# Optimization experiments

Measured on AMD Instinct MI355X. Metric: run time of the kernel, lower is better.

Reference implementation:

```python
import jax, jax.numpy as jnp
import numpy as np

NEG_BIG = -9e15

def setup_inputs() -> dict:
    key = jax.random.key(0)
    k1, k2, k3, k4 = jax.random.split(key, 4)
    B, N, C, D = 8, 2048, 128, 128
    x = jax.random.normal(k1, (B, N, C), dtype=jnp.float32)
    adj = jax.random.randint(k2, (N, N), 0, 2, dtype=jnp.int32)
    W = jax.random.normal(k3, (D, C), dtype=jnp.float32) * (1.0 / np.sqrt(C))
    a = jax.random.normal(k4, (1, 2 * D), dtype=jnp.float32) * (1.0 / np.sqrt(2 * D))
    return {"x": x, "adj": adj, "W": W, "a": a}

def reference(x, adj, W, a):
    # Wh: [B,N,D]
    Wh = jnp.einsum('bnc,dc->bnd', x, W)
    D = Wh.shape[-1]
    a1, a2 = a[0, :D], a[0, D:]
    # e[b,i,j] = leakyrelu(a1.Wh_i + a2.Wh_j)  (algebraic split of cat([Wh_i,Wh_j]) @ a)
    f1 = Wh @ a1  # [B,N]
    f2 = Wh @ a2  # [B,N]
    e = jax.nn.leaky_relu(f1[:, :, None] + f2[:, None, :], negative_slope=0.2)  # [B,N,N]
    e = jnp.where(adj[None] > 0, e, NEG_BIG)
    attention = jax.nn.softmax(e, axis=-1)
    h_prime = jnp.einsum('bij,bjd->bid', attention, Wh)
    return jax.nn.elu(h_prime)
```

## Files before the change

kernel.cpp:

```cpp
#include <hip/hip_runtime.h>
#include <hip/hip_bf16.h>
#include <math.h>

#define BB 8
#define NN 2048
#define CC 128
#define DD 128

typedef __attribute__((ext_vector_type(8))) short short8;
typedef __attribute__((ext_vector_type(4))) float f32x4;

static __device__ __forceinline__ unsigned short f2bf(float f) {
    __hip_bfloat16 h = __float2bfloat16(f);
    return *reinterpret_cast<unsigned short*>(&h);
}
static __device__ __forceinline__ float bf2f(unsigned short u) {
    __hip_bfloat16 h = *reinterpret_cast<__hip_bfloat16*>(&u);
    return __bfloat162float(h);
}

#define PACKB 256
__global__ __launch_bounds__(256) void prep_wh_kernel(
    const int* __restrict__ adj, unsigned int* __restrict__ padj,
    const float* __restrict__ x, const float* __restrict__ W,
    const float* __restrict__ a,
    unsigned short* __restrict__ WhbT,
    float* __restrict__ f1, float* __restrict__ E2g, float* __restrict__ G2g)
{
    __shared__ unsigned short Whs[128 * 136];
    __shared__ unsigned short Wls[128 * 136];
    const int bx  = blockIdx.x;
    const int tid = threadIdx.x;

    if (bx < PACKB) {
        const int wid = bx * 256 + tid;
        #pragma unroll
        for (int rep = 0; rep < 2; ++rep) {
            const int word = wid + rep * 65536;
            const int4* src = (const int4*)adj + (size_t)word * 8;
            unsigned int m = 0;
            #pragma unroll
            for (int k = 0; k < 8; ++k) {
                int4 v = src[k];
                m |= (v.x > 0 ? 1u : 0u) << (k * 4);
                m |= (v.y > 0 ? 1u : 0u) << (k * 4 + 1);
                m |= (v.z > 0 ? 1u : 0u) << (k * 4 + 2);
                m |= (v.w > 0 ? 1u : 0u) << (k * 4 + 3);
            }
            padj[word] = m;
        }
        return;
    }

    const int g  = bx - PACKB;
    const int b  = g & 7;
    const int n0 = (g >> 3) * 64;

    #pragma unroll
    for (int k = 0; k < 16; ++k) {
        const int e   = tid + 256 * k;
        float4 wv = *(const float4*)&W[e * 4];
        const int row = e >> 5;
        const int col = (e & 31) * 4;
        ushort4 hv, lv;
        hv.x = f2bf(wv.x); lv.x = f2bf(wv.x - bf2f(hv.x));
        hv.y = f2bf(wv.y); lv.y = f2bf(wv.y - bf2f(hv.y));
        hv.z = f2bf(wv.z); lv.z = f2bf(wv.z - bf2f(hv.z));
        hv.w = f2bf(wv.w); lv.w = f2bf(wv.w - bf2f(hv.w));
        *(ushort4*)&Whs[row * 136 + col] = hv;
        *(ushort4*)&Wls[row * 136 + col] = lv;
    }
    __syncthreads();

    const int w    = tid >> 6;
    const int lane = tid & 63;
    const int fr   = lane & 15, fk = lane >> 4;
    const int n    = n0 + w * 16 + fr;

    short8 bh[4], bl[4];
    const float* xrow = &x[((size_t)(b * NN) + n) * CC];
    #pragma unroll
    for (int ks = 0; ks < 4; ++ks) {
        float xv[8];
        *(float4*)&xv[0] = *(const float4*)&xrow[(ks * 4 + fk) * 8];
        *(float4*)&xv[4] = *(const float4*)&xrow[(ks * 4 + fk) * 8 + 4];
        #pragma unroll
        for (int e = 0; e < 8; ++e) {
            unsigned short h = f2bf(xv[e]);
            bh[ks][e] = (short)h;
            bl[ks][e] = (short)f2bf(xv[e] - bf2f(h));
        }
    }

    f32x4 acc[8];
    #pragma unroll
    for (int dt = 0; dt < 8; ++dt) acc[dt] = (f32x4){0.f, 0.f, 0.f, 0.f};

    #pragma unroll
    for (int dt = 0; dt < 8; ++dt) {
        #pragma unroll
        for (int ks = 0; ks < 4; ++ks) {
            const int off = (dt * 16 + fr) * 136 + (ks * 4 + fk) * 8;
            short8 aH = *(const short8*)&Whs[off];
            short8 aL = *(const short8*)&Wls[off];
            acc[dt] = __builtin_amdgcn_mfma_f32_16x16x32_bf16(aH, bh[ks], acc[dt], 0, 0, 0);
            acc[dt] = __builtin_amdgcn_mfma_f32_16x16x32_bf16(aH, bl[ks], acc[dt], 0, 0, 0);
            acc[dt] = __builtin_amdgcn_mfma_f32_16x16x32_bf16(aL, bh[ks], acc[dt], 0, 0, 0);
        }
    }

    float p1 = 0.f, p2 = 0.f;
    #pragma unroll
    for (int dt = 0; dt < 8; ++dt) {
        #pragma unroll
        for (int r = 0; r < 4; ++r) {
            const int d = dt * 16 + fk * 4 + r;
            p1 += acc[dt][r] * a[d];
            p2 += acc[dt][r] * a[DD + d];
        }
    }
    p1 += __shfl_xor(p1, 16); p1 += __shfl_xor(p1, 32);
    p2 += __shfl_xor(p2, 16); p2 += __shfl_xor(p2, 32);
    if (fk == 0) {
        f1[b * NN + n]  = p1;
        E2g[b * NN + n] = __expf(p2);
        G2g[b * NN + n] = __expf(0.2f * p2);
    }

    #pragma unroll
    for (int dt = 0; dt < 8; ++dt) {
        #pragma unroll
        for (int r = 0; r < 4; ++r) {
            const int d = dt * 16 + fk * 4 + r;
            WhbT[((size_t)(b * 128 + d)) * NN + n] = f2bf(acc[dt][r]);
        }
    }
}

__global__ __launch_bounds__(512) void gat_kernel(
    const unsigned short* __restrict__ WhbT,
    const unsigned int* __restrict__ padj,
    const float* __restrict__ f1,
    const float* __restrict__ E2g, const float* __restrict__ G2g,
    float* __restrict__ out)
{
    constexpr int NC = NN / 64;
    __shared__ __align__(16) unsigned char smem[66048];
    unsigned short* Bs0 = (unsigned short*)smem;
    unsigned short* Bs1 = (unsigned short*)(smem + 16384);
    unsigned short* Ps0 = (unsigned short*)(smem + 32768);
    unsigned short* Ps1 = (unsigned short*)(smem + 40960);
    float* E2s  = (float*)(smem + 49152);
    float* G2s  = (float*)(smem + 57344);
    float* Srow = (float*)(smem + 65536);
    float* Sred = (float*)(smem + 65792);
    float* T    = (float*)smem;

    const int tid  = threadIdx.x;
    const int gblk = blockIdx.x;
    const int b    = gblk & 7;
    const int i0   = (gblk >> 3) * 64;

    #pragma unroll
    for (int k = 0; k < NN / 512; ++k) {
        E2s[tid + 512 * k] = E2g[b * NN + tid + 512 * k];
        G2s[tid + 512 * k] = G2g[b * NN + tid + 512 * k];
    }

    const int prow = tid >> 3;
    const int pjb  = tid & 7;
    const float f1r = f1[b * NN + i0 + prow];
    const float E1r = __expf(f1r);
    const float G1r = __expf(0.2f * f1r);
    const int psw = ((pjb ^ (prow & 7)) << 3);
    const unsigned int* padjRow = padj + (size_t)(i0 + prow) * 64;

    const int w    = tid >> 6;
    const int wr   = w >> 2, wc = w & 3;
    const int lane = tid & 63;
    const int fr   = lane & 15;
    const int fk   = lane >> 4;
    f32x4 acc00 = {0.f,0.f,0.f,0.f}, acc01 = {0.f,0.f,0.f,0.f};
    f32x4 acc10 = {0.f,0.f,0.f,0.f}, acc11 = {0.f,0.f,0.f,0.f};
    float s_part = 0.f;

    const size_t wbase = (size_t)b * 128 * NN;
    const int g0 = tid,       gd0 = g0 >> 3, gj0 = (g0 & 7) * 8;
    const int g1 = tid + 512, gd1 = g1 >> 3, gj1 = (g1 & 7) * 8;
    const int sw0 = gd0 * 64 + ((((g0) & 7) ^ (gd0 & 7)) << 3);
    const int sw1 = gd1 * 64 + ((((g1) & 7) ^ (gd1 & 7)) << 3);

    uint4 brA0, brA1, brB0, brB1;
    unsigned int pwA, pwB;

#define LOADSET(s, c) do {                                                   \
        br##s##0 = *(const uint4*)&WhbT[wbase + (size_t)gd0 * NN + (c) * 64 + gj0]; \
        br##s##1 = *(const uint4*)&WhbT[wbase + (size_t)gd1 * NN + (c) * 64 + gj1]; \
        pw##s    = padjRow[(c) * 2 + (pjb >> 2)];                            \
    } while (0)

#define PSTAGE(Bsb, Psb, s, c) do {                                          \
        float4 eA = *(const float4*)&E2s[(c) * 64 + pjb * 8];                \
        float4 eB = *(const float4*)&E2s[(c) * 64 + pjb * 8 + 4];            \
        float4 gA = *(const float4*)&G2s[(c) * 64 + pjb * 8];                \
        float4 gB = *(const float4*)&G2s[(c) * 64 + pjb * 8 + 4];            \
        float ev[8], gv[8];                                                  \
        *(float4*)&ev[0] = eA; *(float4*)&ev[4] = eB;                        \
        *(float4*)&gv[0] = gA; *(float4*)&gv[4] = gB;                        \
        unsigned int pbits = (pw##s >> ((pjb & 3) << 3)) & 0xffu;            \
        unsigned short pks[8];                                               \
        float ssum = 0.f;                                                    \
        _Pragma("unroll")                                                    \
        for (int e = 0; e < 8; ++e) {                                        \
            float mv = E1r * ev[e];                                          \
            float gg = G1r * gv[e];                                          \
            float wv = fmaxf(mv, gg);                                        \
            wv = ((pbits >> e) & 1u) ? wv : 0.f;                             \
            unsigned short bw = f2bf(wv);                                    \
            pks[e] = bw;                                                     \
            ssum += bf2f(bw);                                                \
        }                                                                    \
        s_part += ssum;                                                      \
        *(uint4*)&Bsb[sw0] = br##s##0;                                       \
        *(uint4*)&Bsb[sw1] = br##s##1;                                       \
        uint4 pv;                                                            \
        pv.x = (unsigned int)pks[0] | ((unsigned int)pks[1] << 16);          \
        pv.y = (unsigned int)pks[2] | ((unsigned int)pks[3] << 16);          \
        pv.z = (unsigned int)pks[4] | ((unsigned int)pks[5] << 16);          \
        pv.w = (unsigned int)pks[6] | ((unsigned int)pks[7] << 16);          \
        *(uint4*)&Psb[prow * 64 + psw] = pv;                                 \
    } while (0)

#define MFMAC(Bsb, Psb) do {                                                 \
        __builtin_amdgcn_s_setprio(1);                                       \
        _Pragma("unroll")                                                    \
        for (int ks = 0; ks < 2; ++ks) {                                     \
            const int jbl = ks * 4 + fk;                                     \
            const int sb  = ((jbl ^ (fr & 7)) << 3);                         \
            short8 aF0 = *(const short8*)&Psb[(wr * 32 + fr) * 64 + sb];     \
            short8 aF1 = *(const short8*)&Psb[(wr * 32 + 16 + fr) * 64 + sb];\
            short8 bF0 = *(const short8*)&Bsb[(wc * 32 + fr) * 64 + sb];     \
            short8 bF1 = *(const short8*)&Bsb[(wc * 32 + 16 + fr) * 64 + sb];\
            acc00 = __builtin_amdgcn_mfma_f32_16x16x32_bf16(aF0, bF0, acc00, 0, 0, 0); \
            acc01 = __builtin_amdgcn_mfma_f32_16x16x32_bf16(aF0, bF1, acc01, 0, 0, 0); \
            acc10 = __builtin_amdgcn_mfma_f32_16x16x32_bf16(aF1, bF0, acc10, 0, 0, 0); \
            acc11 = __builtin_amdgcn_mfma_f32_16x16x32_bf16(aF1, bF1, acc11, 0, 0, 0); \
        }                                                                    \
        __builtin_amdgcn_s_setprio(0);                                       \
    } while (0)

    LOADSET(A, 0);
    __syncthreads();
    PSTAGE(Bs0, Ps0, A, 0);
    LOADSET(B, 1);
    __syncthreads();

    #pragma unroll 1
    for (int cc = 0; cc < NC; cc += 2) {
        PSTAGE(Bs1, Ps1, B, cc + 1);
        if (cc + 2 < NC) LOADSET(A, cc + 2);
        MFMAC(Bs0, Ps0);
        __syncthreads();
        if (cc + 2 < NC) PSTAGE(Bs0, Ps0, A, cc + 2);
        if (cc + 3 < NC) LOADSET(B, cc + 3);
        MFMAC(Bs1, Ps1);
        __syncthreads();
    }

#undef LOADSET
#undef PSTAGE
#undef MFMAC

    {
        float v = s_part;
        v += __shfl_xor(v, 1); v += __shfl_xor(v, 2); v += __shfl_xor(v, 4);
        if (pjb == 0) Srow[prow] = v;
    }
    __syncthreads();
    if (tid < 64) Sred[tid] = 1.0f / Srow[tid];
    __syncthreads();

    #pragma unroll
    for (int it = 0; it < 2; ++it) {
        #pragma unroll
        for (int dt = 0; dt < 2; ++dt) {
            f32x4 av = (it == 0) ? (dt == 0 ? acc00 : acc01)
                                 : (dt == 0 ? acc10 : acc11);
            #pragma unroll
            for (int r = 0; r < 4; ++r) {
                const int i = wr * 32 + it * 16 + fk * 4 + r;
                const int d = wc * 32 + dt * 16 + fr;
                float hv = av[r] * Sred[i];
                hv = (hv > 0.f) ? hv : expm1f(hv);
                T[i * 132 + d] = hv;
            }
        }
    }
    __syncthreads();

    #pragma unroll
    for (int k = 0; k < 4; ++k) {
        const int g   = tid + 512 * k;
        const int row = g >> 5;
        const int d4  = (g & 31) * 4;
        float4 h = *(const float4*)&T[row * 132 + d4];
        *(float4*)&out[((size_t)(b * NN) + i0 + row) * DD + d4] = h;
    }
}

extern "C" void kernel_launch(void* const* d_in, const int* in_sizes, int n_in,
                              void* d_out, int out_size, void* d_ws, size_t ws_size,
                              hipStream_t stream) {
    const float* x   = (const float*)d_in[0];
    const int*   adj = (const int*)d_in[1];
    const float* W   = (const float*)d_in[2];
    const float* a   = (const float*)d_in[3];
    float* out = (float*)d_out;

    char* p = (char*)d_ws;
    unsigned short* WhbT = (unsigned short*)p; p += (size_t)BB * NN * DD * 2;
    float* f1  = (float*)p; p += (size_t)BB * NN * 4;
    float* E2g = (float*)p; p += (size_t)BB * NN * 4;
    float* G2g = (float*)p; p += (size_t)BB * NN * 4;
    unsigned int* padj = (unsigned int*)p;    p += (size_t)NN * 64 * 4;

    prep_wh_kernel<<<PACKB + (NN / 64) * BB, 256, 0, stream>>>(
        adj, padj, x, W, a, WhbT, f1, E2g, G2g);
    gat_kernel<<<(NN / 64) * BB, 512, 0, stream>>>(
        WhbT, padj, f1, E2g, G2g, out);
}
```

Baseline: 37.02 us.

## Split MFMA K-dimension across warp pairs with wider D tiles per warp

Repartitions the 8 warps from a 2x4 (rows x D) grid into 2 row groups x 2 D halves x 2 K halves. Each warp now covers 64 D columns and only half of each 64-wide K chunk, so one set of A fragments feeds 8 MFMAs per chunk instead of reloading per k-step. The aim is fewer LDS fragment loads per MFMA. In exchange it adds a cross-warp reduction through shared memory in the epilogue, uses more accumulator registers, and folds the normalisation into a division.

```diff
diff --git a/kernel.cpp b/kernel.cpp
--- a/kernel.cpp
+++ b/kernel.cpp
@@ -153,7 +153,6 @@
     float* E2s  = (float*)(smem + 49152);
     float* G2s  = (float*)(smem + 57344);
     float* Srow = (float*)(smem + 65536);
-    float* Sred = (float*)(smem + 65792);
     float* T    = (float*)smem;
 
     const int tid  = threadIdx.x;
@@ -176,12 +175,19 @@
     const unsigned int* padjRow = padj + (size_t)(i0 + prow) * 64;
 
     const int w    = tid >> 6;
-    const int wr   = w >> 2, wc = w & 3;
+    const int wr   = w >> 2;
+    const int wc   = (w >> 1) & 1;
+    const int kh   = w & 1;
     const int lane = tid & 63;
     const int fr   = lane & 15;
     const int fk   = lane >> 4;
-    f32x4 acc00 = {0.f,0.f,0.f,0.f}, acc01 = {0.f,0.f,0.f,0.f};
-    f32x4 acc10 = {0.f,0.f,0.f,0.f}, acc11 = {0.f,0.f,0.f,0.f};
+    const int sbK  = (((kh * 4 + fk) ^ (fr & 7)) << 3);
+    f32x4 acc0[4], acc1[4];
+    #pragma unroll
+    for (int dt = 0; dt < 4; ++dt) {
+        acc0[dt] = (f32x4){0.f,0.f,0.f,0.f};
+        acc1[dt] = (f32x4){0.f,0.f,0.f,0.f};
+    }
     float s_part = 0.f;
 
     const size_t wbase = (size_t)b * 128 * NN;
@@ -233,19 +239,20 @@
 
 #define MFMAC(Bsb, Psb) do {                                                 \
         __builtin_amdgcn_s_setprio(1);                                       \
-        _Pragma("unroll")                                                    \
-        for (int ks = 0; ks < 2; ++ks) {                                     \
-            const int jbl = ks * 4 + fk;                                     \
-            const int sb  = ((jbl ^ (fr & 7)) << 3);                         \
-            short8 aF0 = *(const short8*)&Psb[(wr * 32 + fr) * 64 + sb];     \
-            short8 aF1 = *(const short8*)&Psb[(wr * 32 + 16 + fr) * 64 + sb];\
-            short8 bF0 = *(const short8*)&Bsb[(wc * 32 + fr) * 64 + sb];     \
-            short8 bF1 = *(const short8*)&Bsb[(wc * 32 + 16 + fr) * 64 + sb];\
-            acc00 = __builtin_amdgcn_mfma_f32_16x16x32_bf16(aF0, bF0, acc00, 0, 0, 0); \
-            acc01 = __builtin_amdgcn_mfma_f32_16x16x32_bf16(aF0, bF1, acc01, 0, 0, 0); \
-            acc10 = __builtin_amdgcn_mfma_f32_16x16x32_bf16(aF1, bF0, acc10, 0, 0, 0); \
-            acc11 = __builtin_amdgcn_mfma_f32_16x16x32_bf16(aF1, bF1, acc11, 0, 0, 0); \
-        }                                                                    \
+        short8 aF0 = *(const short8*)&Psb[(wr * 32 + fr) * 64 + sbK];        \
+        short8 aF1 = *(const short8*)&Psb[(wr * 32 + 16 + fr) * 64 + sbK];   \
+        short8 bF0 = *(const short8*)&Bsb[(wc * 64 +      fr) * 64 + sbK];   \
+        short8 bF1 = *(const short8*)&Bsb[(wc * 64 + 16 + fr) * 64 + sbK];   \
+        short8 bF2 = *(const short8*)&Bsb[(wc * 64 + 32 + fr) * 64 + sbK];   \
+        short8 bF3 = *(const short8*)&Bsb[(wc * 64 + 48 + fr) * 64 + sbK];   \
+        acc0[0] = __builtin_amdgcn_mfma_f32_16x16x32_bf16(aF0, bF0, acc0[0], 0, 0, 0); \
+        acc0[1] = __builtin_amdgcn_mfma_f32_16x16x32_bf16(aF0, bF1, acc0[1], 0, 0, 0); \
+        acc0[2] = __builtin_amdgcn_mfma_f32_16x16x32_bf16(aF0, bF2, acc0[2], 0, 0, 0); \
+        acc0[3] = __builtin_amdgcn_mfma_f32_16x16x32_bf16(aF0, bF3, acc0[3], 0, 0, 0); \
+        acc1[0] = __builtin_amdgcn_mfma_f32_16x16x32_bf16(aF1, bF0, acc1[0], 0, 0, 0); \
+        acc1[1] = __builtin_amdgcn_mfma_f32_16x16x32_bf16(aF1, bF1, acc1[1], 0, 0, 0); \
+        acc1[2] = __builtin_amdgcn_mfma_f32_16x16x32_bf16(aF1, bF2, acc1[2], 0, 0, 0); \
+        acc1[3] = __builtin_amdgcn_mfma_f32_16x16x32_bf16(aF1, bF3, acc1[3], 0, 0, 0); \
         __builtin_amdgcn_s_setprio(0);                                       \
     } while (0)
 
@@ -276,23 +283,38 @@
         v += __shfl_xor(v, 1); v += __shfl_xor(v, 2); v += __shfl_xor(v, 4);
         if (pjb == 0) Srow[prow] = v;
     }
-    __syncthreads();
-    if (tid < 64) Sred[tid] = 1.0f / Srow[tid];
-    __syncthreads();
-
-    #pragma unroll
-    for (int it = 0; it < 2; ++it) {
-        #pragma unroll
-        for (int dt = 0; dt < 2; ++dt) {
-            f32x4 av = (it == 0) ? (dt == 0 ? acc00 : acc01)
-                                 : (dt == 0 ? acc10 : acc11);
+
+    if (kh) {
+        #pragma unroll
+        for (int it = 0; it < 2; ++it) {
             #pragma unroll
-            for (int r = 0; r < 4; ++r) {
-                const int i = wr * 32 + it * 16 + fk * 4 + r;
-                const int d = wc * 32 + dt * 16 + fr;
-                float hv = av[r] * Sred[i];
-                hv = (hv > 0.f) ? hv : expm1f(hv);
-                T[i * 132 + d] = hv;
+            for (int dt = 0; dt < 4; ++dt) {
+                f32x4 av = it ? acc1[dt] : acc0[dt];
+                #pragma unroll
+                for (int r = 0; r < 4; ++r) {
+                    const int i = wr * 32 + it * 16 + fk * 4 + r;
+                    const int d = wc * 64 + dt * 16 + fr;
+                    T[i * 132 + d] = av[r];
+                }
+            }
+        }
+    }
+    __syncthreads();
+
+    if (!kh) {
+        #pragma unroll
+        for (int it = 0; it < 2; ++it) {
+            #pragma unroll
+            for (int dt = 0; dt < 4; ++dt) {
+                f32x4 av = it ? acc1[dt] : acc0[dt];
+                #pragma unroll
+                for (int r = 0; r < 4; ++r) {
+                    const int i = wr * 32 + it * 16 + fk * 4 + r;
+                    const int d = wc * 64 + dt * 16 + fr;
+                    float hv = (av[r] + T[i * 132 + d]) / Srow[i];
+                    hv = (hv > 0.f) ? hv : expm1f(hv);
+                    T[i * 132 + d] = hv;
+                }
             }
         }
     }
```

New measurement: 39.83 us. +7.6%, slower.
